# Optimization experiments

Measured on AMD Instinct MI355X. Metric: run time of the kernel, lower is better.

## Reference

```python
import jax, jax.numpy as jnp
import numpy as np

N, DIM, S = 500000, 128, 10
INV_SQRT_2PI = 0.3989422804014327  # 1/sqrt(2*pi)


def _pdf(x, mu, sigma):
    # scipy.stats.norm.pdf(x, loc=mu, scale=sigma)
    z = (x - mu) / sigma
    return (INV_SQRT_2PI / sigma) * jnp.exp(-0.5 * z * z)


def setup_inputs() -> dict:
    key = jax.random.key(0)
    k1, k2, k3 = jax.random.split(key, 3)
    return {
        "encoded": jax.random.normal(k1, (N, DIM), dtype=jnp.float32),
        "normal_dist": jax.random.uniform(k2, (DIM, S), dtype=jnp.float32),
        "anomaly_dist": jax.random.uniform(k3, (DIM, S), dtype=jnp.float32),
    }


def reference(encoded, normal_dist, anomaly_dist):
    dim = encoded.shape[-1]
    # per-dimension mean / unbiased std over the 10 reference samples (torch defaults)
    mu_n = normal_dist.mean(axis=1)            # [DIM]
    sd_n = jnp.std(normal_dist, axis=1, ddof=1)
    mu_a = anomaly_dist.mean(axis=1)
    sd_a = jnp.std(anomaly_dist, axis=1, ddof=1)

    # per-row summed pdf over feature dims (vectorized over batch)
    s_n = _pdf(encoded, mu_n, sd_n).sum(axis=-1)  # [N]
    s_a = _pdf(encoded, mu_a, sd_a).sum(axis=-1)  # [N]

    # faithful carry-over recurrence from the original loop:
    # p_k = (p_{k-1} + s_k) / dim   (pdf_norm/pdf_anom never reset per row)
    inv_dim = jnp.float32(1.0 / dim)

    def step(carry, s):
        pn, pa = carry
        pn = (pn + s[0]) * inv_dim
        pa = (pa + s[1]) * inv_dim
        return (pn, pa), (pn, pa)

    init = (jnp.float32(0.0), jnp.float32(0.0))
    _, (pns, pas) = jax.lax.scan(step, init, (s_n, s_a))

    total = pns + pas
    return jnp.stack([pns / total, pas / total], axis=-1)  # [N, 2]
```

## Files before the change

### kernel.cpp

```cpp
#include <hip/hip_runtime.h>

#define DIM  128
#define SREF 10
#define WREC 8

__global__ void stats_kernel(const float* __restrict__ nd,
                             const float* __restrict__ ad,
                             float* __restrict__ params) {
    int d = threadIdx.x;
    if (d >= DIM) return;
    const float INV_SQRT_2PI = 0.3989422804014327f;

    {
        float v[SREF]; float s = 0.f;
        #pragma unroll
        for (int j = 0; j < SREF; ++j) { v[j] = nd[d * SREF + j]; s += v[j]; }
        float mu = s * (1.0f / SREF);
        float var = 0.f;
        #pragma unroll
        for (int j = 0; j < SREF; ++j) { float t = v[j] - mu; var = fmaf(t, t, var); }
        var *= (1.0f / (SREF - 1));
        float sd = sqrtf(var);
        params[d]           = mu;
        params[DIM + d]     = -0.5f / var;
        params[2 * DIM + d] = INV_SQRT_2PI / sd;
    }
    {
        float v[SREF]; float s = 0.f;
        #pragma unroll
        for (int j = 0; j < SREF; ++j) { v[j] = ad[d * SREF + j]; s += v[j]; }
        float mu = s * (1.0f / SREF);
        float var = 0.f;
        #pragma unroll
        for (int j = 0; j < SREF; ++j) { float t = v[j] - mu; var = fmaf(t, t, var); }
        var *= (1.0f / (SREF - 1));
        float sd = sqrtf(var);
        params[3 * DIM + d] = mu;
        params[4 * DIM + d] = -0.5f / var;
        params[5 * DIM + d] = INV_SQRT_2PI / sd;
    }
}

__global__ __launch_bounds__(256) void score_kernel(const float* __restrict__ enc,
                                                    const float* __restrict__ params,
                                                    float2* __restrict__ s_out,
                                                    int n_rows) {
    const int lane = threadIdx.x & 31;
    const int row  = blockIdx.x * 8 + (threadIdx.x >> 5);

    const float4* p4 = (const float4*)params;
    const float4 mu_n = p4[       lane];
    const float4 b_n  = p4[ 32 +  lane];
    const float4 c_n  = p4[ 64 +  lane];
    const float4 mu_a = p4[ 96 +  lane];
    const float4 b_a  = p4[128 +  lane];
    const float4 c_a  = p4[160 +  lane];

    if (row >= n_rows) return;

    const float4 x = ((const float4*)enc)[row * 32 + lane];

    float sn = 0.f, sa = 0.f;
#define PDF_ACC(comp)                                                          \
    {                                                                          \
        float dn = x.comp - mu_n.comp;                                         \
        sn = fmaf(c_n.comp, __expf(b_n.comp * dn * dn), sn);                   \
        float da = x.comp - mu_a.comp;                                         \
        sa = fmaf(c_a.comp, __expf(b_a.comp * da * da), sa);                   \
    }
    PDF_ACC(x) PDF_ACC(y) PDF_ACC(z) PDF_ACC(w)
#undef PDF_ACC

    #pragma unroll
    for (int m = 16; m >= 1; m >>= 1) {
        sn += __shfl_xor(sn, m, 32);
        sa += __shfl_xor(sa, m, 32);
    }
    if (lane == 0) s_out[row] = make_float2(sn, sa);
}

__global__ __launch_bounds__(256) void finalize_kernel(const float2* __restrict__ s,
                                                       float2* __restrict__ out,
                                                       int n) {
    int i = blockIdx.x * blockDim.x + threadIdx.x;
    if (i >= n) return;
    const float inv_dim = 1.0f / 128.0f;
    float pn = 0.f, pa = 0.f;
    int k0 = i - (WREC - 1);
    if (k0 < 0) k0 = 0;
    for (int k = k0; k <= i; ++k) {
        float2 sv = s[k];
        pn = (pn + sv.x) * inv_dim;
        pa = (pa + sv.y) * inv_dim;
    }
    float tot = pn + pa;
    out[i] = make_float2(pn / tot, pa / tot);
}

extern "C" void kernel_launch(void* const* d_in, const int* in_sizes, int n_in,
                              void* d_out, int out_size, void* d_ws, size_t ws_size,
                              hipStream_t stream) {
    const float* enc = (const float*)d_in[0];
    const float* nd  = (const float*)d_in[1];
    const float* ad  = (const float*)d_in[2];
    const int n_rows = in_sizes[0] / DIM;

    float*  params = (float*)d_ws;
    float2* s_buf  = (float2*)((char*)d_ws + 6 * DIM * sizeof(float));

    stats_kernel<<<1, DIM, 0, stream>>>(nd, ad, params);
    score_kernel<<<(n_rows + 7) / 8, 256, 0, stream>>>(enc, params, s_buf, n_rows);
    finalize_kernel<<<(n_rows + 255) / 256, 256, 0, stream>>>(s_buf, (float2*)d_out, n_rows);
}
```

Before: 354.2 us.

## Fuse stats, scoring and recurrence into one kernel with halo rows

Merges the three kernels into a single launch: each block computes the per-dimension Gaussian parameters into shared memory, scores 64 output rows plus a 7-row halo, and applies the 8-step truncated recurrence from shared memory. This removes two kernel launches and the intermediate score buffer round-trip through global memory, and gives each thread several independent row loads. In exchange, halo rows are read and scored twice and every block recomputes the parameter statistics.

```diff
diff --git a/kernel.cpp b/kernel.cpp
--- a/kernel.cpp
+++ b/kernel.cpp
@@ -2,53 +2,56 @@
 
 #define DIM  128
 #define SREF 10
-#define WREC 8
+#define ROWS_OUT 64
+#define NPASS 9
+#define ROWS_CMP (NPASS * 8)
 
-__global__ void stats_kernel(const float* __restrict__ nd,
-                             const float* __restrict__ ad,
-                             float* __restrict__ params) {
-    int d = threadIdx.x;
-    if (d >= DIM) return;
+__global__ __launch_bounds__(256) void fused_kernel(const float* __restrict__ enc,
+                                                    const float* __restrict__ nd,
+                                                    const float* __restrict__ ad,
+                                                    float2* __restrict__ out,
+                                                    int n) {
+    __shared__ float4 p4[6 * 32];
+    __shared__ float2 sc[ROWS_CMP];
+
+    const int tid = threadIdx.x;
     const float INV_SQRT_2PI = 0.3989422804014327f;
 
-    {
-        float v[SREF]; float s = 0.f;
-        #pragma unroll
-        for (int j = 0; j < SREF; ++j) { v[j] = nd[d * SREF + j]; s += v[j]; }
-        float mu = s * (1.0f / SREF);
-        float var = 0.f;
-        #pragma unroll
-        for (int j = 0; j < SREF; ++j) { float t = v[j] - mu; var = fmaf(t, t, var); }
-        var *= (1.0f / (SREF - 1));
-        float sd = sqrtf(var);
-        params[d]           = mu;
-        params[DIM + d]     = -0.5f / var;
-        params[2 * DIM + d] = INV_SQRT_2PI / sd;
+    if (tid < DIM) {
+        float* pf = (float*)p4;
+        {
+            float v[SREF]; float s = 0.f;
+            #pragma unroll
+            for (int j = 0; j < SREF; ++j) { v[j] = nd[tid * SREF + j]; s += v[j]; }
+            float mu = s * (1.0f / SREF);
+            float var = 0.f;
+            #pragma unroll
+            for (int j = 0; j < SREF; ++j) { float t = v[j] - mu; var = fmaf(t, t, var); }
+            var *= (1.0f / (SREF - 1));
+            pf[tid]           = mu;
+            pf[DIM + tid]     = -0.5f / var;
+            pf[2 * DIM + tid] = INV_SQRT_2PI / sqrtf(var);
+        }
+        {
+            float v[SREF]; float s = 0.f;
+            #pragma unroll
+            for (int j = 0; j < SREF; ++j) { v[j] = ad[tid * SREF + j]; s += v[j]; }
+            float mu = s * (1.0f / SREF);
+            float var = 0.f;
+            #pragma unroll
+            for (int j = 0; j < SREF; ++j) { float t = v[j] - mu; var = fmaf(t, t, var); }
+            var *= (1.0f / (SREF - 1));
+            pf[3 * DIM + tid] = mu;
+            pf[4 * DIM + tid] = -0.5f / var;
+            pf[5 * DIM + tid] = INV_SQRT_2PI / sqrtf(var);
+        }
     }
-    {
-        float v[SREF]; float s = 0.f;
-        #pragma unroll
-        for (int j = 0; j < SREF; ++j) { v[j] = ad[d * SREF + j]; s += v[j]; }
-        float mu = s * (1.0f / SREF);
-        float var = 0.f;
-        #pragma unroll
-        for (int j = 0; j < SREF; ++j) { float t = v[j] - mu; var = fmaf(t, t, var); }
-        var *= (1.0f / (SREF - 1));
-        float sd = sqrtf(var);
-        params[3 * DIM + d] = mu;
-        params[4 * DIM + d] = -0.5f / var;
-        params[5 * DIM + d] = INV_SQRT_2PI / sd;
-    }
-}
+    __syncthreads();
 
-__global__ __launch_bounds__(256) void score_kernel(const float* __restrict__ enc,
-                                                    const float* __restrict__ params,
-                                                    float2* __restrict__ s_out,
-                                                    int n_rows) {
-    const int lane = threadIdx.x & 31;
-    const int row  = blockIdx.x * 8 + (threadIdx.x >> 5);
+    const int lane = tid & 31;
+    const int slot = tid >> 5;
+    const int base = blockIdx.x * ROWS_OUT;
 
-    const float4* p4 = (const float4*)params;
     const float4 mu_n = p4[       lane];
     const float4 b_n  = p4[ 32 +  lane];
     const float4 c_n  = p4[ 64 +  lane];
@@ -56,45 +59,47 @@
     const float4 b_a  = p4[128 +  lane];
     const float4 c_a  = p4[160 +  lane];
 
-    if (row >= n_rows) return;
+    #pragma unroll
+    for (int p = 0; p < NPASS; ++p) {
+        const int idx = p * 8 + slot;
+        const long g = (long)base - 7 + idx;
+        float sn = 0.f, sa = 0.f;
+        if (g >= 0 && g < n) {
+            const float4 x = ((const float4*)enc)[g * 32 + lane];
+#define PDF_ACC(comp)                                                          \
+            {                                                                  \
+                float dn = x.comp - mu_n.comp;                                 \
+                sn = fmaf(c_n.comp, __expf(b_n.comp * dn * dn), sn);           \
+                float da = x.comp - mu_a.comp;                                 \
+                sa = fmaf(c_a.comp, __expf(b_a.comp * da * da), sa);           \
+            }
+            PDF_ACC(x) PDF_ACC(y) PDF_ACC(z) PDF_ACC(w)
+#undef PDF_ACC
+        }
+        #pragma unroll
+        for (int m = 16; m >= 1; m >>= 1) {
+            sn += __shfl_xor(sn, m, 32);
+            sa += __shfl_xor(sa, m, 32);
+        }
+        if (lane == 0) sc[idx] = make_float2(sn, sa);
+    }
+    __syncthreads();
 
-    const float4 x = ((const float4*)enc)[row * 32 + lane];
-
-    float sn = 0.f, sa = 0.f;
-#define PDF_ACC(comp)                                                          \
-    {                                                                          \
-        float dn = x.comp - mu_n.comp;                                         \
-        sn = fmaf(c_n.comp, __expf(b_n.comp * dn * dn), sn);                   \
-        float da = x.comp - mu_a.comp;                                         \
-        sa = fmaf(c_a.comp, __expf(b_a.comp * da * da), sa);                   \
+    if (tid < ROWS_OUT) {
+        const int r = base + tid;
+        if (r < n) {
+            const float inv_dim = 1.0f / 128.0f;
+            float pn = 0.f, pa = 0.f;
+            #pragma unroll
+            for (int k = 0; k < 8; ++k) {
+                const float2 sv = sc[tid + k];
+                pn = (pn + sv.x) * inv_dim;
+                pa = (pa + sv.y) * inv_dim;
+            }
+            const float tot = pn + pa;
+            out[r] = make_float2(pn / tot, pa / tot);
+        }
     }
-    PDF_ACC(x) PDF_ACC(y) PDF_ACC(z) PDF_ACC(w)
-#undef PDF_ACC
-
-    #pragma unroll
-    for (int m = 16; m >= 1; m >>= 1) {
-        sn += __shfl_xor(sn, m, 32);
-        sa += __shfl_xor(sa, m, 32);
-    }
-    if (lane == 0) s_out[row] = make_float2(sn, sa);
-}
-
-__global__ __launch_bounds__(256) void finalize_kernel(const float2* __restrict__ s,
-                                                       float2* __restrict__ out,
-                                                       int n) {
-    int i = blockIdx.x * blockDim.x + threadIdx.x;
-    if (i >= n) return;
-    const float inv_dim = 1.0f / 128.0f;
-    float pn = 0.f, pa = 0.f;
-    int k0 = i - (WREC - 1);
-    if (k0 < 0) k0 = 0;
-    for (int k = k0; k <= i; ++k) {
-        float2 sv = s[k];
-        pn = (pn + sv.x) * inv_dim;
-        pa = (pa + sv.y) * inv_dim;
-    }
-    float tot = pn + pa;
-    out[i] = make_float2(pn / tot, pa / tot);
 }
 
 extern "C" void kernel_launch(void* const* d_in, const int* in_sizes, int n_in,
@@ -105,10 +110,6 @@
     const float* ad  = (const float*)d_in[2];
     const int n_rows = in_sizes[0] / DIM;
 
-    float*  params = (float*)d_ws;
-    float2* s_buf  = (float2*)((char*)d_ws + 6 * DIM * sizeof(float));
-
-    stats_kernel<<<1, DIM, 0, stream>>>(nd, ad, params);
-    score_kernel<<<(n_rows + 7) / 8, 256, 0, stream>>>(enc, params, s_buf, n_rows);
-    finalize_kernel<<<(n_rows + 255) / 256, 256, 0, stream>>>(s_buf, (float2*)d_out, n_rows);
+    fused_kernel<<<(n_rows + ROWS_OUT - 1) / ROWS_OUT, 256, 0, stream>>>(
+        enc, nd, ad, (float2*)d_out, n_rows);
 }
```

Result: faster. 345.6 us (-2.4%).
